# Kernel optimization log

Measured on AMD Instinct MI355X. Metric: run time of the kernel, lower is better.

Reference implementation:

```python
import jax, jax.numpy as jnp
import numpy as np

B, S, T = 8, 32, 64
V = S * T        # 2048 flattened variables
P = 512          # prediction points
N = 2 * S        # neighbors per prediction point
I = 256          # input_dim
H, AD = 8, 32    # attn_heads, attn_dim
D = H * AD       # 256
M = 256          # mlp hidden dim
L = 2            # attn layers
R = 128          # resolution


def setup_inputs() -> dict:
    ks = iter(jax.random.split(jax.random.key(0), 64))
    def w(shape):
        return jax.random.normal(next(ks), shape, jnp.float32) / np.sqrt(shape[-2])
    inp = {
        "encoded": jax.random.normal(next(ks), (B, V, I), jnp.float32),
        "true_u": jax.random.uniform(next(ks), (B, V, 1), jnp.float32),
        "attn_mask": jnp.zeros((P, N), jnp.float32),
        "pred_points": jnp.sort(jax.random.randint(next(ks), (P,), 0, V)),
        "neighbor_index": jax.random.randint(next(ks), (P, N), 0, V),
    }
    for p in ("k", "v"):
        inp[p + "W1"] = w((L, H, I + 1, M)); inp[p + "b1"] = jnp.zeros((L, H, M))
        inp[p + "W2"] = w((L, H, M, M));     inp[p + "b2"] = jnp.zeros((L, H, M))
        inp[p + "W3"] = w((L, H, M, AD));    inp[p + "b3"] = jnp.zeros((L, H, AD))
    inp["ds_W"] = w((I, D)); inp["ds_b"] = jnp.zeros((D,))
    inp["ln1_g"] = jnp.ones((L, D)); inp["ln1_b"] = jnp.zeros((L, D))
    inp["ff_W1"] = w((L, D, D)); inp["ff_b1"] = jnp.zeros((L, D))
    inp["ff_W2"] = w((L, D, D)); inp["ff_b2"] = jnp.zeros((L, D))
    inp["ln2_g"] = jnp.ones((L, D)); inp["ln2_b"] = jnp.zeros((L, D))
    inp["de_W1"] = w((D, M)); inp["de_b1"] = jnp.zeros((M,))
    inp["de_W2"] = w((M, M)); inp["de_b2"] = jnp.zeros((M,))
    inp["de_W3"] = w((M, R)); inp["de_b3"] = jnp.zeros((R,))
    return inp


def _ln(x, g, b):
    mu = x.mean(-1, keepdims=True)
    var = ((x - mu) ** 2).mean(-1, keepdims=True)
    return (x - mu) * jax.lax.rsqrt(var + 1e-5) * g + b


def _kv(x, W1, b1, W2, b2, W3, b3):
    # x: [B,V,I+1]; W1: [L,H,I+1,M] -> per-layer per-head MLP, out [L,B,H,V,AD]
    h = jax.nn.relu(jnp.einsum('bvi,lhim->lbhvm', x, W1) + b1[:, None, :, None, :])
    h = jax.nn.relu(jnp.einsum('lbhvm,lhmn->lbhvn', h, W2) + b2[:, None, :, None, :])
    return jnp.einsum('lbhvm,lhmd->lbhvd', h, W3) + b3[:, None, :, None, :]


def _forward(encoded, true_u, attn_mask, kW1, kb1, kW2, kb2, kW3, kb3,
             vW1, vb1, vW2, vb2, vW3, vb3, ds_W, ds_b, ln1_g, ln1_b,
             ff_W1, ff_b1, ff_W2, ff_b2, ln2_g, ln2_b,
             de_W1, de_b1, de_W2, de_b2, de_W3, de_b3,
             pred_points, neighbor_index):
    attn_dim = kW3.shape[-1]
    n_heads = kW1.shape[1]
    merged = jnp.concatenate([encoded, true_u], axis=-1)        # [B,V,I+1]
    keys = _kv(merged, kW1, kb1, kW2, kb2, kW3, kb3)            # [L,B,H,V,d]
    vals = _kv(merged, vW1, vb1, vW2, vb2, vW3, vb3)            # [L,B,H,V,d]

    cur = encoded[:, pred_points, :]                            # [B,P,I]
    att_value = cur @ ds_W + ds_b                               # [B,P,D]
    nb, np_, dd = att_value.shape
    scale = attn_dim ** (-0.5)
    for l in range(keys.shape[0]):
        q = att_value.reshape(nb, np_, n_heads, attn_dim)       # [B,P,H,d]
        nk = keys[l][:, :, neighbor_index, :]                   # [B,H,P,N,d]
        nv = vals[l][:, :, neighbor_index, :]                   # [B,H,P,N,d]
        scores = (jnp.einsum('bphd,bhpnd->bphn', q, nk) - attn_mask[None, :, None, :]) * scale
        wts = jax.nn.softmax(scores, axis=-1)                   # [B,P,H,N]
        att = jnp.einsum('bphn,bhpnd->bphd', wts, nv).reshape(nb, np_, dd)
        att_value = _ln(att_value + att, ln1_g[l], ln1_b[l])
        ff = jax.nn.relu(att_value @ ff_W1[l] + ff_b1[l]) @ ff_W2[l] + ff_b2[l]
        att_value = _ln(att_value + ff, ln2_g[l], ln2_b[l])

    h = jax.nn.relu(att_value @ de_W1 + de_b1)
    h = jax.nn.relu(h @ de_W2 + de_b2)
    logits = h @ de_W3 + de_b3                                  # [B,P,R]
    res = logits.shape[-1]
    target = jnp.clip(jnp.floor(true_u * res).astype(jnp.int32), 0, res - 1)
    target = target[:, pred_points, :]                          # [B,P,1]
    logprob = jnp.log(jnp.float32(res)) + jax.nn.log_softmax(logits, axis=-1)
    picked = jnp.take_along_axis(logprob, target, axis=2)       # [B,P,1]
    return -picked.sum((1, 2))                                  # [B]


def reference(encoded, true_u, attn_mask, kW1, kb1, kW2, kb2, kW3, kb3,
              vW1, vb1, vW2, vb2, vW3, vb3, ds_W, ds_b, ln1_g, ln1_b,
              ff_W1, ff_b1, ff_W2, ff_b2, ln2_g, ln2_b,
              de_W1, de_b1, de_W2, de_b2, de_W3, de_b3,
              pred_points, neighbor_index):
    return _forward(encoded, true_u, attn_mask, kW1, kb1, kW2, kb2, kW3, kb3,
                    vW1, vb1, vW2, vb2, vW3, vb3, ds_W, ds_b, ln1_g, ln1_b,
                    ff_W1, ff_b1, ff_W2, ff_b2, ln2_g, ln2_b,
                    de_W1, de_b1, de_W2, de_b2, de_W3, de_b3,
                    pred_points, neighbor_index)
```

## Files before the change

### kernel.cpp

```cpp
#include <hip/hip_runtime.h>
#include <hip/hip_bf16.h>
#include <cstdint>
#include <cstddef>

constexpr int Bc = 8;
constexpr int Vc = 2048;
constexpr int Pc = 512;
constexpr int Hc = 8;
constexpr int Lc = 2;
constexpr int ROWS_KV = Bc * Vc;
constexpr int ROWS_AT = Bc * Pc;

typedef __attribute__((ext_vector_type(8))) short bf16x8;
typedef __attribute__((ext_vector_type(4))) float f32x4;

static __device__ __forceinline__ unsigned short f2bf(float v) {
    __hip_bfloat16 h = __float2bfloat16(v);
    return *(unsigned short*)&h;
}
static __device__ __forceinline__ float bf2f(unsigned short u) {
    unsigned int x = ((unsigned int)u) << 16;
    return __uint_as_float(x);
}
static __device__ __forceinline__ float bflo(unsigned int u) {
    return __uint_as_float(u << 16);
}
static __device__ __forceinline__ float bfhi(unsigned int u) {
    return __uint_as_float(u & 0xffff0000u);
}

__global__ __launch_bounds__(256) void conv_x_kernel(
    const float* __restrict__ x, unsigned short* __restrict__ xb)
{
    const int i = blockIdx.x * 256 + threadIdx.x;
    float4 v = ((const float4*)x)[i];
    ushort4 o;
    o.x = f2bf(v.x); o.y = f2bf(v.y); o.z = f2bf(v.z); o.w = f2bf(v.w);
    ((ushort4*)xb)[i] = o;
}

__global__ __launch_bounds__(256) void transpose_all_kernel(
    const float* kW1, const float* vW1, const float* kW2, const float* vW2,
    const float* kW3, const float* vW3,
    const float* ds_W, const float* ff_W1, const float* ff_W2,
    const float* de_W1, const float* de_W2, const float* de_W3,
    unsigned short* __restrict__ W1t, unsigned short* __restrict__ W2t,
    unsigned short* __restrict__ W3t, unsigned short* __restrict__ Wm)
{
    const int z = blockIdx.z;
    const float* src;
    unsigned short* dst;
    int C;
    if (z < 32) {
        const int net = z;
        src = ((net >> 4) ? vW1 : kW1) + (size_t)(net & 15) * 257 * 256;
        dst = W1t + (size_t)net * 65536;
        C = 256;
    } else if (z < 64) {
        const int net = z - 32;
        src = ((net >> 4) ? vW2 : kW2) + (size_t)(net & 15) * 256 * 256;
        dst = W2t + (size_t)net * 65536;
        C = 256;
    } else if (z < 96) {
        const int net = z - 64;
        src = ((net >> 4) ? vW3 : kW3) + (size_t)(net & 15) * 256 * 32;
        dst = W3t + (size_t)net * 8192;
        C = 32;
    } else {
        const int id = z - 96;
        const float* srcs[8] = {ds_W, ff_W1, ff_W1 + (size_t)65536,
                                ff_W2, ff_W2 + (size_t)65536, de_W1, de_W2, de_W3};
        src = srcs[id];
        dst = Wm + (size_t)id * 65536;
        C = (id == 7) ? 128 : 256;
    }
    if (blockIdx.x * 32 >= C) return;
    __shared__ float t[32][33];
    const int c0 = blockIdx.x * 32, k0 = blockIdx.y * 32;
    const int tx = threadIdx.x & 31, ty = threadIdx.x >> 5;
    #pragma unroll
    for (int i = 0; i < 32; i += 8)
        t[ty + i][tx] = src[(size_t)(k0 + ty + i) * C + (c0 + tx)];
    __syncthreads();
    #pragma unroll
    for (int i = 0; i < 32; i += 8)
        dst[(size_t)(c0 + ty + i) * 256 + (k0 + tx)] = f2bf(t[tx][ty + i]);
}

static __device__ __forceinline__ int hsw_chunk(int row, int ks, int quad) {
    int c = ks * 4 + quad;
    int p = c ^ (row & 31);
    return row * 256 + p * 8;
}
static __device__ __forceinline__ int hsw_elem(int row, int col) {
    int p = (col >> 3) ^ (row & 31);
    return row * 256 + p * 8 + (col & 7);
}

__global__ __launch_bounds__(512, 2) void kv_mfma_kernel(
    const unsigned short* __restrict__ Xbf, const float* __restrict__ true_u,
    const unsigned short* __restrict__ W1t, const unsigned short* __restrict__ W2t,
    const unsigned short* __restrict__ W3t,
    const float* __restrict__ kW1, const float* __restrict__ vW1,
    const float* __restrict__ kb1, const float* __restrict__ kb2, const float* __restrict__ kb3,
    const float* __restrict__ vb1, const float* __restrict__ vb2, const float* __restrict__ vb3,
// ... 71 lines not shown
                *(uint4*)&hbuf[xr * 256 + (c ^ (xr & 31)) * 8] = d;
            }
            if (tid < 64) tub[tid] = true_u[row0 + tid];
        }
        __syncthreads();

        f32x4 acc[4][2];
        #pragma unroll
        for (int rt = 0; rt < 4; ++rt)
            #pragma unroll
            for (int ct = 0; ct < 2; ++ct) acc[rt][ct] = zero;
        #pragma unroll
        for (int ks = 0; ks < 8; ++ks) {
            bf16x8 A[4];
            #pragma unroll
            for (int rt = 0; rt < 4; ++rt)
                A[rt] = *(const bf16x8*)&hbuf[hsw_chunk(rt * 16 + ln, ks, quad)];
            #pragma unroll
            for (int rt = 0; rt < 4; ++rt)
                #pragma unroll
                for (int ct = 0; ct < 2; ++ct)
                    acc[rt][ct] = __builtin_amdgcn_mfma_f32_16x16x32_bf16(A[rt], B1[ks * 2 + ct], acc[rt][ct], 0, 0, 0);
        }
        __syncthreads();
        #pragma unroll
        for (int ct = 0; ct < 2; ++ct) {
            const int col = cb + ct * 16 + ln;
            #pragma unroll
            for (int rt = 0; rt < 4; ++rt)
                #pragma unroll
                for (int r = 0; r < 4; ++r) {
                    const int row = rt * 16 + quad * 4 + r;
                    float v = fmaxf(acc[rt][ct][r] + b1v[ct] + tub[row] * w1f[ct], 0.f);
                    hbuf[hsw_elem(row, col)] = f2bf(v);
                }
        }
        __syncthreads();

        #pragma unroll
        for (int rt = 0; rt < 4; ++rt)
            #pragma unroll
            for (int ct = 0; ct < 2; ++ct) acc[rt][ct] = zero;
        #pragma unroll
        for (int ks = 0; ks < 8; ++ks) {
            bf16x8 A[4];
            #pragma unroll
            for (int rt = 0; rt < 4; ++rt)
                A[rt] = *(const bf16x8*)&hbuf[hsw_chunk(rt * 16 + ln, ks, quad)];
            #pragma unroll
            for (int rt = 0; rt < 4; ++rt)
                #pragma unroll
                for (int ct = 0; ct < 2; ++ct)
                    acc[rt][ct] = __builtin_amdgcn_mfma_f32_16x16x32_bf16(A[rt], B2[ks * 2 + ct], acc[rt][ct], 0, 0, 0);
        }
        __syncthreads();
        #pragma unroll
        for (int ct = 0; ct < 2; ++ct) {
            const int col = cb + ct * 16 + ln;
            #pragma unroll
            for (int rt = 0; rt < 4; ++rt)
                #pragma unroll
                for (int r = 0; r < 4; ++r) {
                    const int row = rt * 16 + quad * 4 + r;
                    hbuf[hsw_elem(row, col)] = f2bf(fmaxf(acc[rt][ct][r] + b2v[ct], 0.f));
                }
        }
        __syncthreads();

        f32x4 acc3 = zero;
        #pragma unroll
        for (int ks = 0; ks < 8; ++ks) {
            bf16x8 A  = *(const bf16x8*)&hbuf[hsw_chunk(rt3 * 16 + ln, ks, quad)];
            bf16x8 Bv = *(const bf16x8*)&w3buf[hsw_chunk(ct3 * 16 + ln, ks, quad)];
            acc3 = __builtin_amdgcn_mfma_f32_16x16x32_bf16(A, Bv, acc3, 0, 0, 0);
        }
        #pragma unroll
        for (int r = 0; r < 4; ++r) {
            const int grow = row0 + rt3 * 16 + quad * 4 + r;
            ob[(size_t)(grow & 2047) * 256 + ct3 * 16 + ln] = f2bf(acc3[r] + b3v);
        }
    }
}

__global__ __launch_bounds__(256) void ds_gemm_kernel(
    const unsigned short* __restrict__ Abf, const unsigned short* __restrict__ Wt,
    const float* __restrict__ bias, float* __restrict__ outF,
    const int* __restrict__ pp)
{
    const int tid = threadIdx.x;
    const int w = tid >> 6, lane = tid & 63;
    const int ln = lane & 15, quad = lane >> 4;
    const int row0 = blockIdx.x * 16;
    const int cb = w * 64;

    const f32x4 zero = {0.f, 0.f, 0.f, 0.f};
    f32x4 acc[4];
    #pragma unroll
    for (int ct = 0; ct < 4; ++ct) acc[ct] = zero;

    int ra = row0 + ln;
    size_t arow = (size_t)(ra >> 9) * Vc + pp[ra & 511];
    const unsigned short* wb = Wt + (size_t)(cb + ln) * 256 + quad * 8;
    #pragma unroll
    for (int ks = 0; ks < 8; ++ks) {
        bf16x8 A = *(const bf16x8*)(Abf + arow * 256 + ks * 32 + quad * 8);
        #pragma unroll
        for (int ct = 0; ct < 4; ++ct) {
            bf16x8 Bv = *(const bf16x8*)(wb + (size_t)ct * 16 * 256 + ks * 32);
            acc[ct] = __builtin_amdgcn_mfma_f32_16x16x32_bf16(A, Bv, acc[ct], 0, 0, 0);
        }
    }
    #pragma unroll
    for (int ct = 0; ct < 4; ++ct) {
        const int col = cb + ct * 16 + ln;
        const float bb = bias[col];
        #pragma unroll
        for (int r = 0; r < 4; ++r)
            outF[(size_t)(row0 + quad * 4 + r) * 256 + col] = acc[ct][r] + bb;
    }
}

__global__ __launch_bounds__(512) void attn_ln_kernel(
    const unsigned short* __restrict__ keys, const unsigned short* __restrict__ vals,
    const int* __restrict__ nbr, const float* __restrict__ mask,
    const float* __restrict__ g, const float* __restrict__ be,
    float* __restrict__ AV, unsigned short* __restrict__ AVbf, const int l)
{
    __shared__ float qs[256];
    __shared__ float wts[8 * 64];
    __shared__ float att_s[256];
    __shared__ int ni[64];
    __shared__ float red[4], red2[4];

    const int bid = blockIdx.x;
    const int row = ((bid & 7) << 9) | (bid >> 3);
    const int b = row >> 9, p = row & 511;
    const int tid = threadIdx.x;
    const int h = tid >> 6, n = tid & 63;

    if (tid < 256) qs[tid] = AV[(size_t)row * 256 + tid];
    if (tid < 64)  ni[tid] = nbr[p * 64 + tid];
    __syncthreads();

    const unsigned short* kvbase = keys + (((size_t)l * Bc + b) * Vc) * 256;
    const unsigned short* vvbase = vals + (((size_t)l * Bc + b) * Vc) * 256;

    {
        const int vi = ni[n];
        const unsigned short* kp = kvbase + (size_t)vi * 256 + h * 32;
        const float* qh = qs + h * 32;
        float s = 0.f;
        #pragma unroll
        for (int j = 0; j < 4; ++j) {
            uint4 u = *(const uint4*)(kp + j * 8);
            const float* q = qh + j * 8;
            s += q[0] * bflo(u.x) + q[1] * bfhi(u.x);
            s += q[2] * bflo(u.y) + q[3] * bfhi(u.y);
            s += q[4] * bflo(u.z) + q[5] * bfhi(u.z);
            s += q[6] * bflo(u.w) + q[7] * bfhi(u.w);
        }
        s = (s - mask[p * 64 + n]) * 0.17677669529663689f;
        float mx = s;
        #pragma unroll
        for (int off = 32; off >= 1; off >>= 1) mx = fmaxf(mx, __shfl_xor(mx, off));
        float e = expf(s - mx);
        float sum = e;
        #pragma unroll
        for (int off = 32; off >= 1; off >>= 1) sum += __shfl_xor(sum, off);
        wts[h * 64 + n] = e / sum;
    }

    {
        const int nb4 = n >> 2, cg8 = (n & 3) * 8;
        float a[8];
        #pragma unroll
        for (int j = 0; j < 8; ++j) a[j] = 0.f;
        #pragma unroll
        for (int pass = 0; pass < 4; ++pass) {
            const int nn = pass * 16 + nb4;
            const float wgt = wts[h * 64 + nn];
            const unsigned short* vp = vvbase + (size_t)ni[nn] * 256 + h * 32 + cg8;
            uint4 u = *(const uint4*)vp;
            a[0] += wgt * bflo(u.x); a[1] += wgt * bfhi(u.x);
            a[2] += wgt * bflo(u.y); a[3] += wgt * bfhi(u.y);
            a[4] += wgt * bflo(u.z); a[5] += wgt * bfhi(u.z);
            a[6] += wgt * bflo(u.w); a[7] += wgt * bfhi(u.w);
        }
        #pragma unroll
        for (int off = 4; off <= 32; off <<= 1)
            #pragma unroll
            for (int j = 0; j < 8; ++j)
                a[j] += __shfl_xor(a[j], off);
        if (nb4 == 0)
            #pragma unroll
            for (int j = 0; j < 8; ++j)
                att_s[h * 32 + cg8 + j] = a[j];
    }
    __syncthreads();

    float x = 0.f;
    if (tid < 256) x = qs[tid] + att_s[tid];
    float s = x;
    #pragma unroll
    for (int off = 32; off >= 1; off >>= 1) s += __shfl_xor(s, off);
    if ((tid & 63) == 0 && tid < 256) red[tid >> 6] = s;
    __syncthreads();
    const float mu = (red[0] + red[1] + red[2] + red[3]) * (1.0f / 256.0f);
    const float dx = x - mu;
    float v = dx * dx;
    #pragma unroll
    for (int off = 32; off >= 1; off >>= 1) v += __shfl_xor(v, off);
    if ((tid & 63) == 0 && tid < 256) red2[tid >> 6] = v;
    __syncthreads();
    if (tid < 256) {
        const float var = (red2[0] + red2[1] + red2[2] + red2[3]) * (1.0f / 256.0f);
        float o = dx * (1.0f / sqrtf(var + 1e-5f)) * g[tid] + be[tid];
        AV[(size_t)row * 256 + tid] = o;
        AVbf[(size_t)row * 256 + tid] = f2bf(o);
    }
}

__global__ __launch_bounds__(256) void ff_fused_kernel(
    const unsigned short* __restrict__ Abf, const float* __restrict__ resF,
    const unsigned short* __restrict__ W1t, const float* __restrict__ b1,
    const unsigned short* __restrict__ W2t, const float* __restrict__ b2,
    const float* __restrict__ g, const float* __restrict__ be,
    float* __restrict__ outF, unsigned short* __restrict__ outB)
{
    __shared__ unsigned short hbuf[16 * 256];
    __shared__ float psum[16][4], psq[16][4];

    const int tid = threadIdx.x;
    const int w = tid >> 6, lane = tid & 63;
    const int ln = lane & 15, quad = lane >> 4;
    const int row0 = blockIdx.x * 16;
    const int cb = w * 64;

    const f32x4 zero = {0.f, 0.f, 0.f, 0.f};
    f32x4 acc[4];

    #pragma unroll
    for (int ct = 0; ct < 4; ++ct) acc[ct] = zero;
    {
        const unsigned short* ab = Abf + ((size_t)row0 + ln) * 256 + quad * 8;
        const unsigned short* wb = W1t + (size_t)(cb + ln) * 256 + quad * 8;
        #pragma unroll
        for (int ks = 0; ks < 8; ++ks) {
            bf16x8 A = *(const bf16x8*)(ab + ks * 32);
            #pragma unroll
            for (int ct = 0; ct < 4; ++ct) {
                bf16x8 Bv = *(const bf16x8*)(wb + (size_t)ct * 16 * 256 + ks * 32);
                acc[ct] = __builtin_amdgcn_mfma_f32_16x16x32_bf16(A, Bv, acc[ct], 0, 0, 0);
            }
        }
    }
    #pragma unroll
    for (int ct = 0; ct < 4; ++ct) {
        const int col = cb + ct * 16 + ln;
        const float bb = b1[col];
        #pragma unroll
        for (int r = 0; r < 4; ++r) {
            const int row = quad * 4 + r;
            hbuf[hsw_elem(row, col)] = f2bf(fmaxf(acc[ct][r] + bb, 0.f));
        }
    }
    __syncthreads();

    #pragma unroll
    for (int ct = 0; ct < 4; ++ct) acc[ct] = zero;
    {
        const unsigned short* wb = W2t + (size_t)(cb + ln) * 256 + quad * 8;
        #pragma unroll
        for (int ks = 0; ks < 8; ++ks) {
            bf16x8 A = *(const bf16x8*)&hbuf[hsw_chunk(ln, ks, quad)];
            #pragma unroll
            for (int ct = 0; ct < 4; ++ct) {
                bf16x8 Bv = *(const bf16x8*)(wb + (size_t)ct * 16 * 256 + ks * 32);
                acc[ct] = __builtin_amdgcn_mfma_f32_16x16x32_bf16(A, Bv, acc[ct], 0, 0, 0);
            }
        }
    }
    float vv[4][4];
    #pragma unroll
    for (int ct = 0; ct < 4; ++ct) {
        const int col = cb + ct * 16 + ln;
        const float bb = b2[col];
        #pragma unroll
        for (int r = 0; r < 4; ++r) {
            const int row = quad * 4 + r;
            float res = resF[(size_t)(row0 + row) * 256 + col];
            vv[ct][r] = acc[ct][r] + bb + res;
        }
    }
    #pragma unroll
    for (int r = 0; r < 4; ++r) {
        float sl = 0.f, ql = 0.f;
        #pragma unroll
        for (int ct = 0; ct < 4; ++ct) { float t = vv[ct][r]; sl += t; ql += t * t; }
        #pragma unroll
        for (int off = 8; off >= 1; off >>= 1) {
            sl += __shfl_xor(sl, off);
            ql += __shfl_xor(ql, off);
        }
        if (ln == 0) {
            const int row = quad * 4 + r;
            psum[row][w] = sl; psq[row][w] = ql;
        }
    }
    __syncthreads();

    #pragma unroll
    for (int r = 0; r < 4; ++r) {
        const int row = quad * 4 + r;
        const float mu = (psum[row][0] + psum[row][1] + psum[row][2] + psum[row][3]) * (1.0f / 256.0f);
        const float eq = (psq[row][0] + psq[row][1] + psq[row][2] + psq[row][3]) * (1.0f / 256.0f);
        const float rstd = 1.0f / sqrtf(fmaxf(eq - mu * mu, 0.f) + 1e-5f);
        #pragma unroll
        for (int ct = 0; ct < 4; ++ct) {
            const int col = cb + ct * 16 + ln;
            float o = (vv[ct][r] - mu) * rstd * g[col] + be[col];
            outF[(size_t)(row0 + row) * 256 + col] = o;
            outB[(size_t)(row0 + row) * 256 + col] = f2bf(o);
        }
    }
}

__global__ __launch_bounds__(256) void de_loss_kernel(
    const unsigned short* __restrict__ Abf,
    const unsigned short* __restrict__ W1t, const float* __restrict__ b1,
    const unsigned short* __restrict__ W2t, const float* __restrict__ b2,
    const unsigned short* __restrict__ W3t, const float* __restrict__ b3,
    const float* __restrict__ true_u, const int* __restrict__ pp,
    float* __restrict__ outp)
{
    __shared__ unsigned short hbuf[16 * 256];
    __shared__ float pmax[16][4], psum[16][4], pxt[16][4];
    __shared__ float rowmax[16];
    __shared__ int tcol[16];

    const int tid = threadIdx.x;
    const int w = tid >> 6, lane = tid & 63;
    const int ln = lane & 15, quad = lane >> 4;
    const int row0 = blockIdx.x * 16;
    const int b = row0 >> 9;

    const f32x4 zero = {0.f, 0.f, 0.f, 0.f};
    f32x4 acc[4];

    #pragma unroll
    for (int ct = 0; ct < 4; ++ct) acc[ct] = zero;
    {
        const unsigned short* ab = Abf + ((size_t)row0 + ln) * 256 + quad * 8;
        const unsigned short* wb = W1t + (size_t)(w * 64 + ln) * 256 + quad * 8;
        #pragma unroll
        for (int ks = 0; ks < 8; ++ks) {
            bf16x8 A = *(const bf16x8*)(ab + ks * 32);
            #pragma unroll
            for (int ct = 0; ct < 4; ++ct) {
                bf16x8 Bv = *(const bf16x8*)(wb + (size_t)ct * 16 * 256 + ks * 32);
                acc[ct] = __builtin_amdgcn_mfma_f32_16x16x32_bf16(A, Bv, acc[ct], 0, 0, 0);
            }
        }
    }
    #pragma unroll
    for (int ct = 0; ct < 4; ++ct) {
        const int col = w * 64 + ct * 16 + ln;
        const float bb = b1[col];
        #pragma unroll
        for (int r = 0; r < 4; ++r) {
            const int row = quad * 4 + r;
            hbuf[hsw_elem(row, col)] = f2bf(fmaxf(acc[ct][r] + bb, 0.f));
        }
    }
    __syncthreads();

    #pragma unroll
    for (int ct = 0; ct < 4; ++ct) acc[ct] = zero;
    {
        const unsigned short* wb = W2t + (size_t)(w * 64 + ln) * 256 + quad * 8;
        #pragma unroll
        for (int ks = 0; ks < 8; ++ks) {
            bf16x8 A = *(const bf16x8*)&hbuf[hsw_chunk(ln, ks, quad)];
            #pragma unroll
            for (int ct = 0; ct < 4; ++ct) {
                bf16x8 Bv = *(const bf16x8*)(wb + (size_t)ct * 16 * 256 + ks * 32);
                acc[ct] = __builtin_amdgcn_mfma_f32_16x16x32_bf16(A, Bv, acc[ct], 0, 0, 0);
            }
        }
    }
    __syncthreads();
    #pragma unroll
    for (int ct = 0; ct < 4; ++ct) {
        const int col = w * 64 + ct * 16 + ln;
        const float bb = b2[col];
        #pragma unroll
        for (int r = 0; r < 4; ++r) {
            const int row = quad * 4 + r;
            hbuf[hsw_elem(row, col)] = f2bf(fmaxf(acc[ct][r] + bb, 0.f));
        }
    }
    __syncthreads();

    const int cb3 = w * 32;
    f32x4 a3[2];
    a3[0] = zero; a3[1] = zero;
    #pragma unroll
    for (int ks = 0; ks < 8; ++ks) {
        bf16x8 A = *(const bf16x8*)&hbuf[hsw_chunk(ln, ks, quad)];
        #pragma unroll
        for (int ct = 0; ct < 2; ++ct) {
            bf16x8 Bv = *(const bf16x8*)(W3t + (size_t)(cb3 + ct * 16 + ln) * 256 + ks * 32 + quad * 8);
            a3[ct] = __builtin_amdgcn_mfma_f32_16x16x32_bf16(A, Bv, a3[ct], 0, 0, 0);
        }
    }
    float lg[2][4];
    #pragma unroll
    for (int ct = 0; ct < 2; ++ct) {
        const float bb = b3[cb3 + ct * 16 + ln];
        #pragma unroll
        for (int r = 0; r < 4; ++r) lg[ct][r] = a3[ct][r] + bb;
    }

    #pragma unroll
    for (int r = 0; r < 4; ++r) {
        float m = fmaxf(lg[0][r], lg[1][r]);
        #pragma unroll
        for (int off = 8; off >= 1; off >>= 1) m = fmaxf(m, __shfl_xor(m, off));
        if (ln == 0) pmax[quad * 4 + r][w] = m;
    }
    __syncthreads();
    if (tid < 16) {
        const int grow = row0 + tid;
        rowmax[tid] = fmaxf(fmaxf(pmax[tid][0], pmax[tid][1]), fmaxf(pmax[tid][2], pmax[tid][3]));
        float tu = true_u[(size_t)(grow >> 9) * Vc + pp[grow & 511]];
        int t = (int)floorf(tu * 128.0f);
        tcol[tid] = t < 0 ? 0 : (t > 127 ? 127 : t);
    }
    __syncthreads();
    #pragma unroll
    for (int r = 0; r < 4; ++r) {
        const int row = quad * 4 + r;
        const float mx = rowmax[row];
        const int t = tcol[row];
        float e = expf(lg[0][r] - mx) + expf(lg[1][r] - mx);
        float xt = ((cb3 + ln) == t ? lg[0][r] : 0.f) +
                   ((cb3 + 16 + ln) == t ? lg[1][r] : 0.f);
        #pragma unroll
        for (int off = 8; off >= 1; off >>= 1) {
            e += __shfl_xor(e, off);
            xt += __shfl_xor(xt, off);
        }
        if (ln == 0) { psum[row][w] = e; pxt[row][w] = xt; }
    }
    __syncthreads();
    float contrib = 0.f;
    if (tid < 16) {
        const float sum = psum[tid][0] + psum[tid][1] + psum[tid][2] + psum[tid][3];
        const float xt  = pxt[tid][0] + pxt[tid][1] + pxt[tid][2] + pxt[tid][3];
        const float lp = logf(128.0f) + (xt - rowmax[tid]) - logf(sum);
        contrib = -lp;
    }
    if (w == 0) {
        #pragma unroll
        for (int off = 32; off >= 1; off >>= 1) contrib += __shfl_xor(contrib, off);
        if (lane == 0) atomicAdd(&outp[b], contrib);
    }
}

extern "C" void kernel_launch(void* const* d_in, const int* in_sizes, int n_in,
                              void* d_out, int out_size, void* d_ws, size_t ws_size,
                              hipStream_t stream)
{
    (void)in_sizes; (void)n_in; (void)out_size; (void)ws_size;

    const float* encoded        = (const float*)d_in[0];
    const float* true_u         = (const float*)d_in[1];
    const float* attn_mask      = (const float*)d_in[2];
    const int*   pred_points    = (const int*)d_in[3];
    const int*   neighbor_index = (const int*)d_in[4];
    const float* kW1 = (const float*)d_in[5];
    const float* kb1 = (const float*)d_in[6];
    const float* kW2 = (const float*)d_in[7];
    const float* kb2 = (const float*)d_in[8];
    const float* kW3 = (const float*)d_in[9];
    const float* kb3 = (const float*)d_in[10];
    const float* vW1 = (const float*)d_in[11];
    const float* vb1 = (const float*)d_in[12];
    const float* vW2 = (const float*)d_in[13];
    const float* vb2 = (const float*)d_in[14];
    const float* vW3 = (const float*)d_in[15];
    const float* vb3 = (const float*)d_in[16];
    const float* ds_W  = (const float*)d_in[17];
    const float* ds_b  = (const float*)d_in[18];
    const float* ln1_g = (const float*)d_in[19];
    const float* ln1_b = (const float*)d_in[20];
    const float* ff_W1 = (const float*)d_in[21];
    const float* ff_b1 = (const float*)d_in[22];
    const float* ff_W2 = (const float*)d_in[23];
    const float* ff_b2 = (const float*)d_in[24];
    const float* ln2_g = (const float*)d_in[25];
    const float* ln2_b = (const float*)d_in[26];
    const float* de_W1 = (const float*)d_in[27];
    const float* de_b1 = (const float*)d_in[28];
    const float* de_W2 = (const float*)d_in[29];
    const float* de_b2 = (const float*)d_in[30];
    const float* de_W3 = (const float*)d_in[31];
    const float* de_b3 = (const float*)d_in[32];

    float* out = (float*)d_out;

    constexpr size_t KV_ELEMS = (size_t)Lc * Bc * Hc * Vc * 32;
    unsigned short* keys = (unsigned short*)d_ws;
    unsigned short* vals = keys + KV_ELEMS;
    float* AV = (float*)(vals + KV_ELEMS);
    unsigned short* Xbf  = (unsigned short*)(AV + (size_t)ROWS_AT * 256);
    unsigned short* W1t  = Xbf + (size_t)ROWS_KV * 256;
    unsigned short* W2t  = W1t + (size_t)32 * 65536;
    unsigned short* W3t  = W2t + (size_t)32 * 65536;
    unsigned short* Wm   = W3t + (size_t)32 * 8192;
    unsigned short* AVbf = Wm + (size_t)8 * 65536;

    (void)hipMemsetAsync(out, 0, Bc * sizeof(float), stream);

    conv_x_kernel<<<dim3(ROWS_KV * 256 / 4 / 256), 256, 0, stream>>>(encoded, Xbf);
    transpose_all_kernel<<<dim3(8, 8, 104), 256, 0, stream>>>(
        kW1, vW1, kW2, vW2, kW3, vW3,
        ds_W, ff_W1, ff_W2, de_W1, de_W2, de_W3,
        W1t, W2t, W3t, Wm);

    kv_mfma_kernel<<<dim3(16, 16, 2), 512, 0, stream>>>(
        Xbf, true_u, W1t, W2t, W3t, kW1, vW1,
        kb1, kb2, kb3, vb1, vb2, vb3, keys, vals);

    ds_gemm_kernel<<<dim3(ROWS_AT / 16), 256, 0, stream>>>(
        Xbf, Wm + (size_t)0 * 65536, ds_b, AV, pred_points);

    for (int l = 0; l < Lc; ++l) {
        attn_ln_kernel<<<dim3(ROWS_AT), 512, 0, stream>>>(
            keys, vals, neighbor_index, attn_mask,
            ln1_g + l * 256, ln1_b + l * 256, AV, AVbf, l);
        ff_fused_kernel<<<dim3(ROWS_AT / 16), 256, 0, stream>>>(
            AVbf, AV,
            Wm + (size_t)(1 + l) * 65536, ff_b1 + l * 256,
            Wm + (size_t)(3 + l) * 65536, ff_b2 + l * 256,
            ln2_g + l * 256, ln2_b + l * 256, AV, AVbf);
    }

    de_loss_kernel<<<dim3(ROWS_AT / 16), 256, 0, stream>>>(
        AVbf,
        Wm + (size_t)5 * 65536, de_b1,
        Wm + (size_t)6 * 65536, de_b2,
        Wm + (size_t)7 * 65536, de_b3,
        true_u, pred_points, out);
}
```

Before: 474.7 us.

## Fuse downsample, attention layers, feed-forward and decoder loss into one kernel

Replaces the six post-KV kernels (ds gemm, per-layer attention+LN and FF, decoder loss) with a single decoder kernel in which each 512-thread block owns 16 prediction rows and keeps activations in shared memory across all stages. This removes the launch gaps and the global round-trips of the fp32 and bf16 activation buffers. The trade-off is parallelism: the attention now runs per wave over 2 rows and 8 heads serially, with only 256 blocks in total, versus one block per row before, so the gather-bound attention may lose latency hiding.

New measurement: 464.9 us. 2.1% less time.

```diff
diff --git a/kernel.cpp b/kernel.cpp
--- a/kernel.cpp
+++ b/kernel.cpp
@@ -17,10 +17,6 @@
 static __device__ __forceinline__ unsigned short f2bf(float v) {
     __hip_bfloat16 h = __float2bfloat16(v);
     return *(unsigned short*)&h;
-}
-static __device__ __forceinline__ float bf2f(unsigned short u) {
-    unsigned int x = ((unsigned int)u) << 16;
-    return __uint_as_float(x);
 }
 static __device__ __forceinline__ float bflo(unsigned int u) {
     return __uint_as_float(u << 16);
@@ -258,388 +254,376 @@
     }
 }
 
-__global__ __launch_bounds__(256) void ds_gemm_kernel(
-    const unsigned short* __restrict__ Abf, const unsigned short* __restrict__ Wt,
-    const float* __restrict__ bias, float* __restrict__ outF,
-    const int* __restrict__ pp)
+__global__ __launch_bounds__(512) void decoder_kernel(
+    const unsigned short* __restrict__ Xbf, const float* __restrict__ true_u,
+    const unsigned short* __restrict__ keys, const unsigned short* __restrict__ vals,
+    const int* __restrict__ nbr, const float* __restrict__ mask,
+    const int* __restrict__ pp, const unsigned short* __restrict__ Wm,
+    const float* __restrict__ ds_b,
+    const float* __restrict__ ln1_g, const float* __restrict__ ln1_b,
+    const float* __restrict__ ff_b1, const float* __restrict__ ff_b2,
+    const float* __restrict__ ln2_g, const float* __restrict__ ln2_b,
+    const float* __restrict__ de_b1, const float* __restrict__ de_b2,
+    const float* __restrict__ de_b3, float* __restrict__ outp)
 {
+    __shared__ float avF[16][264];
+    __shared__ float attF[16][264];
+    __shared__ unsigned short abuf[16 * 256];
+    __shared__ unsigned short hbuf[16 * 256];
+    __shared__ int   ni_s[16][64];
+    __shared__ float wtsb[8][64];
+    __shared__ float psum[16][8], psq[16][8];
+    __shared__ float rowmax[16];
+    __shared__ int   tcol[16];
+    __shared__ int   pps[16];
+
     const int tid = threadIdx.x;
     const int w = tid >> 6, lane = tid & 63;
     const int ln = lane & 15, quad = lane >> 4;
-    const int row0 = blockIdx.x * 16;
-    const int cb = w * 64;
+    const int bid = blockIdx.x;
+    const int b = bid & 7;
+    const int r0 = b * 512 + (bid >> 3) * 16;
+    const int cb = w * 32;
 
     const f32x4 zero = {0.f, 0.f, 0.f, 0.f};
-    f32x4 acc[4];
+
+    if (tid < 16) pps[tid] = pp[(r0 + tid) & 511];
     #pragma unroll
-    for (int ct = 0; ct < 4; ++ct) acc[ct] = zero;
-
-    int ra = row0 + ln;
-    size_t arow = (size_t)(ra >> 9) * Vc + pp[ra & 511];
-    const unsigned short* wb = Wt + (size_t)(cb + ln) * 256 + quad * 8;
-    #pragma unroll
-    for (int ks = 0; ks < 8; ++ks) {
-        bf16x8 A = *(const bf16x8*)(Abf + arow * 256 + ks * 32 + quad * 8);
-        #pragma unroll
-        for (int ct = 0; ct < 4; ++ct) {
-            bf16x8 Bv = *(const bf16x8*)(wb + (size_t)ct * 16 * 256 + ks * 32);
-            acc[ct] = __builtin_amdgcn_mfma_f32_16x16x32_bf16(A, Bv, acc[ct], 0, 0, 0);
-        }
-    }
-    #pragma unroll
-    for (int ct = 0; ct < 4; ++ct) {
-        const int col = cb + ct * 16 + ln;
-        const float bb = bias[col];
-        #pragma unroll
-        for (int r = 0; r < 4; ++r)
-            outF[(size_t)(row0 + quad * 4 + r) * 256 + col] = acc[ct][r] + bb;
-    }
-}
-
-__global__ __launch_bounds__(512) void attn_ln_kernel(
-    const unsigned short* __restrict__ keys, const unsigned short* __restrict__ vals,
-    const int* __restrict__ nbr, const float* __restrict__ mask,
-    const float* __restrict__ g, const float* __restrict__ be,
-    float* __restrict__ AV, unsigned short* __restrict__ AVbf, const int l)
-{
-    __shared__ float qs[256];
-    __shared__ float wts[8 * 64];
-    __shared__ float att_s[256];
-    __shared__ int ni[64];
-    __shared__ float red[4], red2[4];
-
-    const int bid = blockIdx.x;
-    const int row = ((bid & 7) << 9) | (bid >> 3);
-    const int b = row >> 9, p = row & 511;
-    const int tid = threadIdx.x;
-    const int h = tid >> 6, n = tid & 63;
-
-    if (tid < 256) qs[tid] = AV[(size_t)row * 256 + tid];
-    if (tid < 64)  ni[tid] = nbr[p * 64 + tid];
+    for (int j = 0; j < 2; ++j) {
+        const int idx = tid * 2 + j;
+        const int row = idx >> 6, n = idx & 63;
+        ni_s[row][n] = nbr[((r0 + row) & 511) * 64 + n];
+    }
     __syncthreads();
 
-    const unsigned short* kvbase = keys + (((size_t)l * Bc + b) * Vc) * 256;
-    const unsigned short* vvbase = vals + (((size_t)l * Bc + b) * Vc) * 256;
-
     {
-        const int vi = ni[n];
-        const unsigned short* kp = kvbase + (size_t)vi * 256 + h * 32;
-        const float* qh = qs + h * 32;
-        float s = 0.f;
-        #pragma unroll
-        for (int j = 0; j < 4; ++j) {
-            uint4 u = *(const uint4*)(kp + j * 8);
-            const float* q = qh + j * 8;
-            s += q[0] * bflo(u.x) + q[1] * bfhi(u.x);
-            s += q[2] * bflo(u.y) + q[3] * bfhi(u.y);
-            s += q[4] * bflo(u.z) + q[5] * bfhi(u.z);
-            s += q[6] * bflo(u.w) + q[7] * bfhi(u.w);
-        }
-        s = (s - mask[p * 64 + n]) * 0.17677669529663689f;
-        float mx = s;
-        #pragma unroll
-        for (int off = 32; off >= 1; off >>= 1) mx = fmaxf(mx, __shfl_xor(mx, off));
-        float e = expf(s - mx);
-        float sum = e;
-        #pragma unroll
-        for (int off = 32; off >= 1; off >>= 1) sum += __shfl_xor(sum, off);
-        wts[h * 64 + n] = e / sum;
-    }
+        const int row = tid >> 5, c = tid & 31;
+        const size_t arow = (size_t)b * Vc + pps[row];
+        uint4 d = *(const uint4*)(Xbf + arow * 256 + c * 8);
+        *(uint4*)&abuf[row * 256 + ((c ^ row) * 8)] = d;
+    }
+    __syncthreads();
 
     {
-        const int nb4 = n >> 2, cg8 = (n & 3) * 8;
-        float a[8];
-        #pragma unroll
-        for (int j = 0; j < 8; ++j) a[j] = 0.f;
-        #pragma unroll
-        for (int pass = 0; pass < 4; ++pass) {
-            const int nn = pass * 16 + nb4;
-            const float wgt = wts[h * 64 + nn];
-            const unsigned short* vp = vvbase + (size_t)ni[nn] * 256 + h * 32 + cg8;
-            uint4 u = *(const uint4*)vp;
-            a[0] += wgt * bflo(u.x); a[1] += wgt * bfhi(u.x);
-            a[2] += wgt * bflo(u.y); a[3] += wgt * bfhi(u.y);
-            a[4] += wgt * bflo(u.z); a[5] += wgt * bfhi(u.z);
-            a[6] += wgt * bflo(u.w); a[7] += wgt * bfhi(u.w);
-        }
-        #pragma unroll
-        for (int off = 4; off <= 32; off <<= 1)
-            #pragma unroll
-            for (int j = 0; j < 8; ++j)
-                a[j] += __shfl_xor(a[j], off);
-        if (nb4 == 0)
-            #pragma unroll
-            for (int j = 0; j < 8; ++j)
-                att_s[h * 32 + cg8 + j] = a[j];
-    }
-    __syncthreads();
-
-    float x = 0.f;
-    if (tid < 256) x = qs[tid] + att_s[tid];
-    float s = x;
-    #pragma unroll
-    for (int off = 32; off >= 1; off >>= 1) s += __shfl_xor(s, off);
-    if ((tid & 63) == 0 && tid < 256) red[tid >> 6] = s;
-    __syncthreads();
-    const float mu = (red[0] + red[1] + red[2] + red[3]) * (1.0f / 256.0f);
-    const float dx = x - mu;
-    float v = dx * dx;
-    #pragma unroll
-    for (int off = 32; off >= 1; off >>= 1) v += __shfl_xor(v, off);
-    if ((tid & 63) == 0 && tid < 256) red2[tid >> 6] = v;
-    __syncthreads();
-    if (tid < 256) {
-        const float var = (red2[0] + red2[1] + red2[2] + red2[3]) * (1.0f / 256.0f);
-        float o = dx * (1.0f / sqrtf(var + 1e-5f)) * g[tid] + be[tid];
-        AV[(size_t)row * 256 + tid] = o;
-        AVbf[(size_t)row * 256 + tid] = f2bf(o);
-    }
-}
-
-__global__ __launch_bounds__(256) void ff_fused_kernel(
-    const unsigned short* __restrict__ Abf, const float* __restrict__ resF,
-    const unsigned short* __restrict__ W1t, const float* __restrict__ b1,
-    const unsigned short* __restrict__ W2t, const float* __restrict__ b2,
-    const float* __restrict__ g, const float* __restrict__ be,
-    float* __restrict__ outF, unsigned short* __restrict__ outB)
-{
-    __shared__ unsigned short hbuf[16 * 256];
-    __shared__ float psum[16][4], psq[16][4];
-
-    const int tid = threadIdx.x;
-    const int w = tid >> 6, lane = tid & 63;
-    const int ln = lane & 15, quad = lane >> 4;
-    const int row0 = blockIdx.x * 16;
-    const int cb = w * 64;
-
-    const f32x4 zero = {0.f, 0.f, 0.f, 0.f};
-    f32x4 acc[4];
-
-    #pragma unroll
-    for (int ct = 0; ct < 4; ++ct) acc[ct] = zero;
-    {
-        const unsigned short* ab = Abf + ((size_t)row0 + ln) * 256 + quad * 8;
-        const unsigned short* wb = W1t + (size_t)(cb + ln) * 256 + quad * 8;
+        const unsigned short* Wt = Wm;
+        f32x4 acc[2]; acc[0] = zero; acc[1] = zero;
+        const unsigned short* wb = Wt + (size_t)(cb + ln) * 256 + quad * 8;
         #pragma unroll
         for (int ks = 0; ks < 8; ++ks) {
-            bf16x8 A = *(const bf16x8*)(ab + ks * 32);
-            #pragma unroll
-            for (int ct = 0; ct < 4; ++ct) {
+            bf16x8 A = *(const bf16x8*)&abuf[hsw_chunk(ln, ks, quad)];
+            #pragma unroll
+            for (int ct = 0; ct < 2; ++ct) {
                 bf16x8 Bv = *(const bf16x8*)(wb + (size_t)ct * 16 * 256 + ks * 32);
                 acc[ct] = __builtin_amdgcn_mfma_f32_16x16x32_bf16(A, Bv, acc[ct], 0, 0, 0);
             }
         }
-    }
-    #pragma unroll
-    for (int ct = 0; ct < 4; ++ct) {
-        const int col = cb + ct * 16 + ln;
-        const float bb = b1[col];
+        __syncthreads();
+        #pragma unroll
+        for (int ct = 0; ct < 2; ++ct) {
+            const int col = cb + ct * 16 + ln;
+            const float bb = ds_b[col];
+            #pragma unroll
+            for (int r = 0; r < 4; ++r) {
+                const int row = quad * 4 + r;
+                float v = acc[ct][r] + bb;
+                avF[row][col] = v;
+                abuf[hsw_elem(row, col)] = f2bf(v);
+            }
+        }
+    }
+    __syncthreads();
+
+    for (int l = 0; l < Lc; ++l) {
+        const unsigned short* kvb = keys + (((size_t)l * Bc + b) * Vc) * 256;
+        const unsigned short* vvb = vals + (((size_t)l * Bc + b) * Vc) * 256;
+
+        #pragma unroll
+        for (int rr = 0; rr < 2; ++rr) {
+            const int row = w * 2 + rr;
+            const int p = (r0 + row) & 511;
+            const int n = lane;
+            for (int h = 0; h < 8; ++h) {
+                float q[32];
+                #pragma unroll
+                for (int j = 0; j < 8; ++j) {
+                    float4 t4 = *(const float4*)&avF[row][h * 32 + j * 4];
+                    q[j * 4 + 0] = t4.x; q[j * 4 + 1] = t4.y;
+                    q[j * 4 + 2] = t4.z; q[j * 4 + 3] = t4.w;
+                }
+                const int vi = ni_s[row][n];
+                const unsigned short* kp = kvb + (size_t)vi * 256 + h * 32;
+                float s = 0.f;
+                #pragma unroll
+                for (int j = 0; j < 4; ++j) {
+                    uint4 u = *(const uint4*)(kp + j * 8);
+                    s += q[j * 8 + 0] * bflo(u.x) + q[j * 8 + 1] * bfhi(u.x);
+                    s += q[j * 8 + 2] * bflo(u.y) + q[j * 8 + 3] * bfhi(u.y);
+                    s += q[j * 8 + 4] * bflo(u.z) + q[j * 8 + 5] * bfhi(u.z);
+                    s += q[j * 8 + 6] * bflo(u.w) + q[j * 8 + 7] * bfhi(u.w);
+                }
+                s = (s - mask[p * 64 + n]) * 0.17677669529663689f;
+                float mx = s;
+                #pragma unroll
+                for (int off = 32; off >= 1; off >>= 1) mx = fmaxf(mx, __shfl_xor(mx, off));
+                float e = expf(s - mx);
+                float sum = e;
+                #pragma unroll
+                for (int off = 32; off >= 1; off >>= 1) sum += __shfl_xor(sum, off);
+                wtsb[w][n] = e / sum;
+                const int nb4 = n >> 2, cg8 = (n & 3) * 8;
+                float a[8];
+                #pragma unroll
+                for (int j = 0; j < 8; ++j) a[j] = 0.f;
+                #pragma unroll
+                for (int pass = 0; pass < 4; ++pass) {
+                    const int nn = pass * 16 + nb4;
+                    const float wgt = wtsb[w][nn];
+                    const unsigned short* vp = vvb + (size_t)ni_s[row][nn] * 256 + h * 32 + cg8;
+                    uint4 u = *(const uint4*)vp;
+                    a[0] += wgt * bflo(u.x); a[1] += wgt * bfhi(u.x);
+                    a[2] += wgt * bflo(u.y); a[3] += wgt * bfhi(u.y);
+                    a[4] += wgt * bflo(u.z); a[5] += wgt * bfhi(u.z);
+                    a[6] += wgt * bflo(u.w); a[7] += wgt * bfhi(u.w);
+                }
+                #pragma unroll
+                for (int off = 4; off <= 32; off <<= 1)
+                    #pragma unroll
+                    for (int j = 0; j < 8; ++j)
+                        a[j] += __shfl_xor(a[j], off);
+                if (nb4 == 0)
+                    #pragma unroll
+                    for (int j = 0; j < 8; ++j)
+                        attF[row][h * 32 + cg8 + j] = a[j];
+            }
+            {
+                const int c0 = lane * 4;
+                float x[4];
+                float sl = 0.f, ql = 0.f;
+                #pragma unroll
+                for (int j = 0; j < 4; ++j) {
+                    x[j] = avF[row][c0 + j] + attF[row][c0 + j];
+                    sl += x[j]; ql += x[j] * x[j];
+                }
+                #pragma unroll
+                for (int off = 32; off >= 1; off >>= 1) {
+                    sl += __shfl_xor(sl, off);
+                    ql += __shfl_xor(ql, off);
+                }
+                const float mu = sl * (1.0f / 256.0f);
+                const float var = ql * (1.0f / 256.0f) - mu * mu;
+                const float rstd = 1.0f / sqrtf(fmaxf(var, 0.f) + 1e-5f);
+                #pragma unroll
+                for (int j = 0; j < 4; ++j) {
+                    const int col = c0 + j;
+                    float o = (x[j] - mu) * rstd * ln1_g[l * 256 + col] + ln1_b[l * 256 + col];
+                    avF[row][col] = o;
+                    abuf[hsw_elem(row, col)] = f2bf(o);
+                }
+            }
+        }
+        __syncthreads();
+
+        {
+            const unsigned short* W1 = Wm + (size_t)(1 + l) * 65536;
+            f32x4 acc[2]; acc[0] = zero; acc[1] = zero;
+            const unsigned short* wb = W1 + (size_t)(cb + ln) * 256 + quad * 8;
+            #pragma unroll
+            for (int ks = 0; ks < 8; ++ks) {
+                bf16x8 A = *(const bf16x8*)&abuf[hsw_chunk(ln, ks, quad)];
+                #pragma unroll
+                for (int ct = 0; ct < 2; ++ct) {
+                    bf16x8 Bv = *(const bf16x8*)(wb + (size_t)ct * 16 * 256 + ks * 32);
+                    acc[ct] = __builtin_amdgcn_mfma_f32_16x16x32_bf16(A, Bv, acc[ct], 0, 0, 0);
+                }
+            }
+            #pragma unroll
+            for (int ct = 0; ct < 2; ++ct) {
+                const int col = cb + ct * 16 + ln;
+                const float bb = ff_b1[l * 256 + col];
+                #pragma unroll
+                for (int r = 0; r < 4; ++r) {
+                    const int row = quad * 4 + r;
+                    hbuf[hsw_elem(row, col)] = f2bf(fmaxf(acc[ct][r] + bb, 0.f));
+                }
+            }
+        }
+        __syncthreads();
+
+        {
+            const unsigned short* W2 = Wm + (size_t)(3 + l) * 65536;
+            f32x4 acc[2]; acc[0] = zero; acc[1] = zero;
+            const unsigned short* wb = W2 + (size_t)(cb + ln) * 256 + quad * 8;
+            #pragma unroll
+            for (int ks = 0; ks < 8; ++ks) {
+                bf16x8 A = *(const bf16x8*)&hbuf[hsw_chunk(ln, ks, quad)];
+                #pragma unroll
+                for (int ct = 0; ct < 2; ++ct) {
+                    bf16x8 Bv = *(const bf16x8*)(wb + (size_t)ct * 16 * 256 + ks * 32);
+                    acc[ct] = __builtin_amdgcn_mfma_f32_16x16x32_bf16(A, Bv, acc[ct], 0, 0, 0);
+                }
+            }
+            float vv[2][4];
+            #pragma unroll
+            for (int ct = 0; ct < 2; ++ct) {
+                const int col = cb + ct * 16 + ln;
+                const float bb = ff_b2[l * 256 + col];
+                #pragma unroll
+                for (int r = 0; r < 4; ++r) {
+                    const int row = quad * 4 + r;
+                    vv[ct][r] = acc[ct][r] + bb + avF[row][col];
+                }
+            }
+            #pragma unroll
+            for (int r = 0; r < 4; ++r) {
+                float sl = vv[0][r] + vv[1][r];
+                float ql = vv[0][r] * vv[0][r] + vv[1][r] * vv[1][r];
+                #pragma unroll
+                for (int off = 8; off >= 1; off >>= 1) {
+                    sl += __shfl_xor(sl, off);
+                    ql += __shfl_xor(ql, off);
+                }
+                if (ln == 0) {
+                    const int row = quad * 4 + r;
+                    psum[row][w] = sl; psq[row][w] = ql;
+                }
+            }
+            __syncthreads();
+            #pragma unroll
+            for (int r = 0; r < 4; ++r) {
+                const int row = quad * 4 + r;
+                float sl = 0.f, ql = 0.f;
+                #pragma unroll
+                for (int j = 0; j < 8; ++j) { sl += psum[row][j]; ql += psq[row][j]; }
+                const float mu = sl * (1.0f / 256.0f);
+                const float var = ql * (1.0f / 256.0f) - mu * mu;
+                const float rstd = 1.0f / sqrtf(fmaxf(var, 0.f) + 1e-5f);
+                #pragma unroll
+                for (int ct = 0; ct < 2; ++ct) {
+                    const int col = cb + ct * 16 + ln;
+                    float o = (vv[ct][r] - mu) * rstd * ln2_g[l * 256 + col] + ln2_b[l * 256 + col];
+                    avF[row][col] = o;
+                    abuf[hsw_elem(row, col)] = f2bf(o);
+                }
+            }
+        }
+        __syncthreads();
+    }
+
+    {
+        const unsigned short* W1 = Wm + (size_t)5 * 65536;
+        f32x4 acc[2]; acc[0] = zero; acc[1] = zero;
+        const unsigned short* wb = W1 + (size_t)(cb + ln) * 256 + quad * 8;
+        #pragma unroll
+        for (int ks = 0; ks < 8; ++ks) {
+            bf16x8 A = *(const bf16x8*)&abuf[hsw_chunk(ln, ks, quad)];
+            #pragma unroll
+            for (int ct = 0; ct < 2; ++ct) {
+                bf16x8 Bv = *(const bf16x8*)(wb + (size_t)ct * 16 * 256 + ks * 32);
+                acc[ct] = __builtin_amdgcn_mfma_f32_16x16x32_bf16(A, Bv, acc[ct], 0, 0, 0);
+            }
+        }
+        #pragma unroll
+        for (int ct = 0; ct < 2; ++ct) {
+            const int col = cb + ct * 16 + ln;
+            const float bb = de_b1[col];
+            #pragma unroll
+            for (int r = 0; r < 4; ++r) {
+                const int row = quad * 4 + r;
+                hbuf[hsw_elem(row, col)] = f2bf(fmaxf(acc[ct][r] + bb, 0.f));
+            }
+        }
+    }
+    __syncthreads();
+
+    {
+        const unsigned short* W2 = Wm + (size_t)6 * 65536;
+        f32x4 acc[2]; acc[0] = zero; acc[1] = zero;
+        const unsigned short* wb = W2 + (size_t)(cb + ln) * 256 + quad * 8;
+        #pragma unroll
+        for (int ks = 0; ks < 8; ++ks) {
+            bf16x8 A = *(const bf16x8*)&hbuf[hsw_chunk(ln, ks, quad)];
+            #pragma unroll
+            for (int ct = 0; ct < 2; ++ct) {
+                bf16x8 Bv = *(const bf16x8*)(wb + (size_t)ct * 16 * 256 + ks * 32);
+                acc[ct] = __builtin_amdgcn_mfma_f32_16x16x32_bf16(A, Bv, acc[ct], 0, 0, 0);
+            }
+        }
+        __syncthreads();
+        #pragma unroll
+        for (int ct = 0; ct < 2; ++ct) {
+            const int col = cb + ct * 16 + ln;
+            const float bb = de_b2[col];
+            #pragma unroll
+            for (int r = 0; r < 4; ++r) {
+                const int row = quad * 4 + r;
+                hbuf[hsw_elem(row, col)] = f2bf(fmaxf(acc[ct][r] + bb, 0.f));
+            }
+        }
+    }
+    __syncthreads();
+
+    {
+        const unsigned short* W3 = Wm + (size_t)7 * 65536;
+        const int cb3 = w * 16;
+        f32x4 a3 = zero;
+        const unsigned short* wb = W3 + (size_t)(cb3 + ln) * 256 + quad * 8;
+        #pragma unroll
+        for (int ks = 0; ks < 8; ++ks) {
+            bf16x8 A = *(const bf16x8*)&hbuf[hsw_chunk(ln, ks, quad)];
+            bf16x8 Bv = *(const bf16x8*)(wb + ks * 32);
+            a3 = __builtin_amdgcn_mfma_f32_16x16x32_bf16(A, Bv, a3, 0, 0, 0);
+        }
+        float lg[4];
+        const float bb = de_b3[cb3 + ln];
+        #pragma unroll
+        for (int r = 0; r < 4; ++r) lg[r] = a3[r] + bb;
+
+        #pragma unroll
+        for (int r = 0; r < 4; ++r) {
+            float m = lg[r];
+            #pragma unroll
+            for (int off = 8; off >= 1; off >>= 1) m = fmaxf(m, __shfl_xor(m, off));
+            if (ln == 0) psum[quad * 4 + r][w] = m;
+        }
+        __syncthreads();
+        if (tid < 16) {
+            float m = psum[tid][0];
+            #pragma unroll
+            for (int j = 1; j < 8; ++j) m = fmaxf(m, psum[tid][j]);
+            rowmax[tid] = m;
+            float tu = true_u[(size_t)b * Vc + pps[tid]];
+            int t = (int)floorf(tu * 128.0f);
+            tcol[tid] = t < 0 ? 0 : (t > 127 ? 127 : t);
+        }
+        __syncthreads();
         #pragma unroll
         for (int r = 0; r < 4; ++r) {
             const int row = quad * 4 + r;
-            hbuf[hsw_elem(row, col)] = f2bf(fmaxf(acc[ct][r] + bb, 0.f));
-        }
-    }
-    __syncthreads();
-
-    #pragma unroll
-    for (int ct = 0; ct < 4; ++ct) acc[ct] = zero;
-    {
-        const unsigned short* wb = W2t + (size_t)(cb + ln) * 256 + quad * 8;
-        #pragma unroll
-        for (int ks = 0; ks < 8; ++ks) {
-            bf16x8 A = *(const bf16x8*)&hbuf[hsw_chunk(ln, ks, quad)];
-            #pragma unroll
-            for (int ct = 0; ct < 4; ++ct) {
-                bf16x8 Bv = *(const bf16x8*)(wb + (size_t)ct * 16 * 256 + ks * 32);
-                acc[ct] = __builtin_amdgcn_mfma_f32_16x16x32_bf16(A, Bv, acc[ct], 0, 0, 0);
-            }
-        }
-    }
-    float vv[4][4];
-    #pragma unroll
-    for (int ct = 0; ct < 4; ++ct) {
-        const int col = cb + ct * 16 + ln;
-        const float bb = b2[col];
-        #pragma unroll
-        for (int r = 0; r < 4; ++r) {
-            const int row = quad * 4 + r;
-            float res = resF[(size_t)(row0 + row) * 256 + col];
-            vv[ct][r] = acc[ct][r] + bb + res;
-        }
-    }
-    #pragma unroll
-    for (int r = 0; r < 4; ++r) {
-        float sl = 0.f, ql = 0.f;
-        #pragma unroll
-        for (int ct = 0; ct < 4; ++ct) { float t = vv[ct][r]; sl += t; ql += t * t; }
-        #pragma unroll
-        for (int off = 8; off >= 1; off >>= 1) {
-            sl += __shfl_xor(sl, off);
-            ql += __shfl_xor(ql, off);
-        }
-        if (ln == 0) {
-            const int row = quad * 4 + r;
-            psum[row][w] = sl; psq[row][w] = ql;
-        }
-    }
-    __syncthreads();
-
-    #pragma unroll
-    for (int r = 0; r < 4; ++r) {
-        const int row = quad * 4 + r;
-        const float mu = (psum[row][0] + psum[row][1] + psum[row][2] + psum[row][3]) * (1.0f / 256.0f);
-        const float eq = (psq[row][0] + psq[row][1] + psq[row][2] + psq[row][3]) * (1.0f / 256.0f);
-        const float rstd = 1.0f / sqrtf(fmaxf(eq - mu * mu, 0.f) + 1e-5f);
-        #pragma unroll
-        for (int ct = 0; ct < 4; ++ct) {
-            const int col = cb + ct * 16 + ln;
-            float o = (vv[ct][r] - mu) * rstd * g[col] + be[col];
-            outF[(size_t)(row0 + row) * 256 + col] = o;
-            outB[(size_t)(row0 + row) * 256 + col] = f2bf(o);
-        }
-    }
-}
-
-__global__ __launch_bounds__(256) void de_loss_kernel(
-    const unsigned short* __restrict__ Abf,
-    const unsigned short* __restrict__ W1t, const float* __restrict__ b1,
-    const unsigned short* __restrict__ W2t, const float* __restrict__ b2,
-    const unsigned short* __restrict__ W3t, const float* __restrict__ b3,
-    const float* __restrict__ true_u, const int* __restrict__ pp,
-    float* __restrict__ outp)
-{
-    __shared__ unsigned short hbuf[16 * 256];
-    __shared__ float pmax[16][4], psum[16][4], pxt[16][4];
-    __shared__ float rowmax[16];
-    __shared__ int tcol[16];
-
-    const int tid = threadIdx.x;
-    const int w = tid >> 6, lane = tid & 63;
-    const int ln = lane & 15, quad = lane >> 4;
-    const int row0 = blockIdx.x * 16;
-    const int b = row0 >> 9;
-
-    const f32x4 zero = {0.f, 0.f, 0.f, 0.f};
-    f32x4 acc[4];
-
-    #pragma unroll
-    for (int ct = 0; ct < 4; ++ct) acc[ct] = zero;
-    {
-        const unsigned short* ab = Abf + ((size_t)row0 + ln) * 256 + quad * 8;
-        const unsigned short* wb = W1t + (size_t)(w * 64 + ln) * 256 + quad * 8;
-        #pragma unroll
-        for (int ks = 0; ks < 8; ++ks) {
-            bf16x8 A = *(const bf16x8*)(ab + ks * 32);
-            #pragma unroll
-            for (int ct = 0; ct < 4; ++ct) {
-                bf16x8 Bv = *(const bf16x8*)(wb + (size_t)ct * 16 * 256 + ks * 32);
-                acc[ct] = __builtin_amdgcn_mfma_f32_16x16x32_bf16(A, Bv, acc[ct], 0, 0, 0);
-            }
-        }
-    }
-    #pragma unroll
-    for (int ct = 0; ct < 4; ++ct) {
-        const int col = w * 64 + ct * 16 + ln;
-        const float bb = b1[col];
-        #pragma unroll
-        for (int r = 0; r < 4; ++r) {
-            const int row = quad * 4 + r;
-            hbuf[hsw_elem(row, col)] = f2bf(fmaxf(acc[ct][r] + bb, 0.f));
-        }
-    }
-    __syncthreads();
-
-    #pragma unroll
-    for (int ct = 0; ct < 4; ++ct) acc[ct] = zero;
-    {
-        const unsigned short* wb = W2t + (size_t)(w * 64 + ln) * 256 + quad * 8;
-        #pragma unroll
-        for (int ks = 0; ks < 8; ++ks) {
-            bf16x8 A = *(const bf16x8*)&hbuf[hsw_chunk(ln, ks, quad)];
-            #pragma unroll
-            for (int ct = 0; ct < 4; ++ct) {
-                bf16x8 Bv = *(const bf16x8*)(wb + (size_t)ct * 16 * 256 + ks * 32);
-                acc[ct] = __builtin_amdgcn_mfma_f32_16x16x32_bf16(A, Bv, acc[ct], 0, 0, 0);
-            }
-        }
-    }
-    __syncthreads();
-    #pragma unroll
-    for (int ct = 0; ct < 4; ++ct) {
-        const int col = w * 64 + ct * 16 + ln;
-        const float bb = b2[col];
-        #pragma unroll
-        for (int r = 0; r < 4; ++r) {
-            const int row = quad * 4 + r;
-            hbuf[hsw_elem(row, col)] = f2bf(fmaxf(acc[ct][r] + bb, 0.f));
-        }
-    }
-    __syncthreads();
-
-    const int cb3 = w * 32;
-    f32x4 a3[2];
-    a3[0] = zero; a3[1] = zero;
-    #pragma unroll
-    for (int ks = 0; ks < 8; ++ks) {
-        bf16x8 A = *(const bf16x8*)&hbuf[hsw_chunk(ln, ks, quad)];
-        #pragma unroll
-        for (int ct = 0; ct < 2; ++ct) {
-            bf16x8 Bv = *(const bf16x8*)(W3t + (size_t)(cb3 + ct * 16 + ln) * 256 + ks * 32 + quad * 8);
-            a3[ct] = __builtin_amdgcn_mfma_f32_16x16x32_bf16(A, Bv, a3[ct], 0, 0, 0);
-        }
-    }
-    float lg[2][4];
-    #pragma unroll
-    for (int ct = 0; ct < 2; ++ct) {
-        const float bb = b3[cb3 + ct * 16 + ln];
-        #pragma unroll
-        for (int r = 0; r < 4; ++r) lg[ct][r] = a3[ct][r] + bb;
-    }
-
-    #pragma unroll
-    for (int r = 0; r < 4; ++r) {
-        float m = fmaxf(lg[0][r], lg[1][r]);
-        #pragma unroll
-        for (int off = 8; off >= 1; off >>= 1) m = fmaxf(m, __shfl_xor(m, off));
-        if (ln == 0) pmax[quad * 4 + r][w] = m;
-    }
-    __syncthreads();
-    if (tid < 16) {
-        const int grow = row0 + tid;
-        rowmax[tid] = fmaxf(fmaxf(pmax[tid][0], pmax[tid][1]), fmaxf(pmax[tid][2], pmax[tid][3]));
-        float tu = true_u[(size_t)(grow >> 9) * Vc + pp[grow & 511]];
-        int t = (int)floorf(tu * 128.0f);
-        tcol[tid] = t < 0 ? 0 : (t > 127 ? 127 : t);
-    }
-    __syncthreads();
-    #pragma unroll
-    for (int r = 0; r < 4; ++r) {
-        const int row = quad * 4 + r;
-        const float mx = rowmax[row];
-        const int t = tcol[row];
-        float e = expf(lg[0][r] - mx) + expf(lg[1][r] - mx);
-        float xt = ((cb3 + ln) == t ? lg[0][r] : 0.f) +
-                   ((cb3 + 16 + ln) == t ? lg[1][r] : 0.f);
-        #pragma unroll
-        for (int off = 8; off >= 1; off >>= 1) {
-            e += __shfl_xor(e, off);
-            xt += __shfl_xor(xt, off);
-        }
-        if (ln == 0) { psum[row][w] = e; pxt[row][w] = xt; }
-    }
-    __syncthreads();
-    float contrib = 0.f;
-    if (tid < 16) {
-        const float sum = psum[tid][0] + psum[tid][1] + psum[tid][2] + psum[tid][3];
-        const float xt  = pxt[tid][0] + pxt[tid][1] + pxt[tid][2] + pxt[tid][3];
-        const float lp = logf(128.0f) + (xt - rowmax[tid]) - logf(sum);
-        contrib = -lp;
-    }
-    if (w == 0) {
-        #pragma unroll
-        for (int off = 32; off >= 1; off >>= 1) contrib += __shfl_xor(contrib, off);
-        if (lane == 0) atomicAdd(&outp[b], contrib);
+            const float mx = rowmax[row];
+            const int t = tcol[row];
+            float e = expf(lg[r] - mx);
+            float xt = ((cb3 + ln) == t) ? lg[r] : 0.f;
+            #pragma unroll
+            for (int off = 8; off >= 1; off >>= 1) {
+                e += __shfl_xor(e, off);
+                xt += __shfl_xor(xt, off);
+            }
+            if (ln == 0) { psum[row][w] = e; psq[row][w] = xt; }
+        }
+        __syncthreads();
+        float contrib = 0.f;
+        if (tid < 16) {
+            float sum = 0.f, xt = 0.f;
+            #pragma unroll
+            for (int j = 0; j < 8; ++j) { sum += psum[tid][j]; xt += psq[tid][j]; }
+            const float lp = logf(128.0f) + (xt - rowmax[tid]) - logf(sum);
+            contrib = -lp;
+        }
+        if (w == 0) {
+            #pragma unroll
+            for (int off = 32; off >= 1; off >>= 1) contrib += __shfl_xor(contrib, off);
+            if (lane == 0) atomicAdd(&outp[b], contrib);
+        }
     }
 }
 
@@ -688,13 +672,11 @@
     constexpr size_t KV_ELEMS = (size_t)Lc * Bc * Hc * Vc * 32;
     unsigned short* keys = (unsigned short*)d_ws;
     unsigned short* vals = keys + KV_ELEMS;
-    float* AV = (float*)(vals + KV_ELEMS);
-    unsigned short* Xbf  = (unsigned short*)(AV + (size_t)ROWS_AT * 256);
+    unsigned short* Xbf  = vals + KV_ELEMS;
     unsigned short* W1t  = Xbf + (size_t)ROWS_KV * 256;
     unsigned short* W2t  = W1t + (size_t)32 * 65536;
     unsigned short* W3t  = W2t + (size_t)32 * 65536;
     unsigned short* Wm   = W3t + (size_t)32 * 8192;
-    unsigned short* AVbf = Wm + (size_t)8 * 65536;
 
     (void)hipMemsetAsync(out, 0, Bc * sizeof(float), stream);
 
@@ -708,24 +690,8 @@
         Xbf, true_u, W1t, W2t, W3t, kW1, vW1,
         kb1, kb2, kb3, vb1, vb2, vb3, keys, vals);
 
-    ds_gemm_kernel<<<dim3(ROWS_AT / 16), 256, 0, stream>>>(
-        Xbf, Wm + (size_t)0 * 65536, ds_b, AV, pred_points);
-
-    for (int l = 0; l < Lc; ++l) {
-        attn_ln_kernel<<<dim3(ROWS_AT), 512, 0, stream>>>(
-            keys, vals, neighbor_index, attn_mask,
-            ln1_g + l * 256, ln1_b + l * 256, AV, AVbf, l);
-        ff_fused_kernel<<<dim3(ROWS_AT / 16), 256, 0, stream>>>(
-            AVbf, AV,
-            Wm + (size_t)(1 + l) * 65536, ff_b1 + l * 256,
-            Wm + (size_t)(3 + l) * 65536, ff_b2 + l * 256,
-            ln2_g + l * 256, ln2_b + l * 256, AV, AVbf);
-    }
-
-    de_loss_kernel<<<dim3(ROWS_AT / 16), 256, 0, stream>>>(
-        AVbf,
-        Wm + (size_t)5 * 65536, de_b1,
-        Wm + (size_t)6 * 65536, de_b2,
-        Wm + (size_t)7 * 65536, de_b3,
-        true_u, pred_points, out);
-}
+    decoder_kernel<<<dim3(ROWS_AT / 16), 512, 0, stream>>>(
+        Xbf, true_u, keys, vals, neighbor_index, attn_mask, pred_points, Wm,
+        ds_b, ln1_g, ln1_b, ff_b1, ff_b2, ln2_g, ln2_b,
+        de_b1, de_b2, de_b3, out);
+}
```
